# Kernel tuning notes

Hardware: AMD Instinct MI355X
Metric: run time of the kernel (lower is better)

Reference implementation:

```python
import jax, jax.numpy as jnp
import numpy as np
import math


def setup_inputs() -> dict:
    key = jax.random.key(0)
    ks = jax.random.split(key, 5)
    B, C, E = 4, 2048, 1024
    max_len = 2048
    s = 1.0 / math.sqrt(E)
    return {
        "x": jax.random.normal(ks[0], (B, C, E), dtype=jnp.float32),
        "W_q": jax.random.normal(ks[1], (E, E), dtype=jnp.float32) * s,
        "W_k": jax.random.normal(ks[2], (E, E), dtype=jnp.float32) * s,
        "W_v": jax.random.normal(ks[3], (E, E), dtype=jnp.float32) * s,
        "rel_bias": jax.random.normal(ks[4], (2 * max_len - 1, 1), dtype=jnp.float32),
        "max_len": max_len,
    }


def reference(x, W_q, W_k, W_v, rel_bias, max_len):
    B, C, E = x.shape
    # nn.Linear(bias=False): y = x @ W.T
    Q = jnp.einsum("bce,fe->bcf", x, W_q)
    K = jnp.einsum("bce,fe->bcf", x, W_k)
    V = jnp.einsum("bce,fe->bcf", x, W_v)
    scores = jnp.einsum("bqe,bke->bqk", Q, K) / math.sqrt(E)
    pos = jnp.arange(C)
    rel_dist = jnp.clip(pos[None, :] - pos[:, None] + (max_len - 1), 0, 2 * max_len - 2)
    bias = rel_bias[rel_dist, 0]  # [C, C]
    scores = scores + bias[None, :, :]
    weights = jax.nn.softmax(scores, axis=-1)
    out = jnp.einsum("bqk,bke->bqe", weights, V)
    return out, weights
```

## Files before the change

kernel.cpp:

```cpp
#include <hip/hip_runtime.h>
#include <hip/hip_bf16.h>
#include <math.h>

typedef __attribute__((ext_vector_type(8))) short short8;
typedef __attribute__((ext_vector_type(4))) short short4v;
typedef __attribute__((ext_vector_type(4))) float f32x4;

static __device__ __forceinline__ short f2bf(float f) {
  union { float f; unsigned u; } x;
  x.f = f;
  unsigned r = x.u + 0x7fffu + ((x.u >> 16) & 1u);
  return (short)(r >> 16);
}

#define GLD16(g, l)                                                   \
  __builtin_amdgcn_global_load_lds(                                   \
      (const __attribute__((address_space(1))) void*)(g),             \
      (__attribute__((address_space(3))) void*)(l), 16, 0, 0)
#define BAR() asm volatile("s_barrier" ::: "memory")
#define VMCNT6() asm volatile("s_waitcnt vmcnt(6)" ::: "memory")
#define VMCNT0() asm volatile("s_waitcnt vmcnt(0)" ::: "memory")

__global__ __launch_bounds__(256) void cvt_f32_bf16(const float* __restrict__ in,
                                                    short* __restrict__ out, int n8) {
  int i = blockIdx.x * 256 + threadIdx.x;
  if (i >= n8) return;
  const float4* p = (const float4*)in + (size_t)i * 2;
  float4 a = p[0], b = p[1];
  short8 o;
  o[0] = f2bf(a.x); o[1] = f2bf(a.y); o[2] = f2bf(a.z); o[3] = f2bf(a.w);
  o[4] = f2bf(b.x); o[5] = f2bf(b.y); o[6] = f2bf(b.z); o[7] = f2bf(b.w);
  *((short8*)out + i) = o;
}

template <int MODE>
__global__ __launch_bounds__(512) void gemm3b(
    const short* __restrict__ A, const short* __restrict__ Bt,
    void* __restrict__ C0, void* __restrict__ C1, void* __restrict__ C2,
    const float* __restrict__ rel_bias,
    int N, int K, long aZ, long bZ, long cZ, int Cdim, float scale, int ml) {
  __shared__ short sA[3][256 * 64];
  __shared__ short sB[3][128 * 64];
  const int tid = threadIdx.x, lane = tid & 63, wid = tid >> 6;
  const int z = blockIdx.z;
  const short* Az = A + (size_t)z * aZ;
  const short* Bz = Bt + (size_t)z * bZ;
  const int brow = blockIdx.x * 256, bcol = blockIdx.y * 128;
  const int wr = wid >> 2, wc = wid & 3;
  const int lrow = lane & 15, kg = lane >> 4;
  const int l8 = lane >> 3, lm8 = lane & 7;
  const int scol = (lm8 ^ l8) * 8;

  const short* aS[2][2];
  int aD[2][2];
#pragma unroll
  for (int h = 0; h < 2; ++h)
#pragma unroll
    for (int j = 0; j < 2; ++j) {
      int c = wid * 2 + j;
      int rb = c * 8 + (c >= 8 ? 64 : 0) + h * 64;
      aS[h][j] = Az + (size_t)(brow + rb + l8) * K + scol;
      aD[h][j] = rb * 64;
    }
  const short* bS[2];
  int bD[2];
#pragma unroll
  for (int h = 0; h < 2; ++h) {
    int rb = wid * 8 + h * 64;
    bS[h] = Bz + (size_t)(bcol + rb + l8) * K + scol;
    bD[h] = rb * 64;
  }

  const int sks0 = ((0 + kg) ^ (lrow & 7)) * 8;
  const int sks1 = ((4 + kg) ^ (lrow & 7)) * 8;
  const int aR = (wr * 128 + lrow) * 64;
  const int bR = (wc * 32 + lrow) * 64;

  short8 a[4][2], b[2][2];
  f32x4 acc[8][2] = {};

  short *pa0 = &sA[0][0], *pa1 = &sA[1][0], *pa2 = &sA[2][0];
  short *pb0 = &sB[0][0], *pb1 = &sB[1][0], *pb2 = &sB[2][0];

#define STG_A(PA, H, T)                                          \
  do {                                                           \
    GLD16(aS[H][0] + (size_t)(T) * 64, (PA) + aD[H][0]);         \
    GLD16(aS[H][1] + (size_t)(T) * 64, (PA) + aD[H][1]);         \
  } while (0)
#define STG_B(PB, H, T) GLD16(bS[H] + (size_t)(T) * 64, (PB) + bD[H])
#define RD_A(PA, MH)                                                          \
  do {                                                                        \
    _Pragma("unroll") for (int mq = 0; mq < 4; ++mq) {                        \
      a[mq][0] = *(const short8*)&(PA)[aR + (MH)*4096 + mq * 1024 + sks0];    \
      a[mq][1] = *(const short8*)&(PA)[aR + (MH)*4096 + mq * 1024 + sks1];    \
    }                                                                         \
  } while (0)
#define RD_B(PB)                                                   \
  do {                                                             \
    _Pragma("unroll") for (int nq = 0; nq < 2; ++nq) {             \
      b[nq][0] = *(const short8*)&(PB)[bR + nq * 1024 + sks0];     \
      b[nq][1] = *(const short8*)&(PB)[bR + nq * 1024 + sks1];     \
    }                                                              \
  } while (0)
#define MFMA16(MH)                                                            \
  do {                                                                        \
    __builtin_amdgcn_s_setprio(1);                                            \
    _Pragma("unroll") for (int mq = 0; mq < 4; ++mq)                          \
        _Pragma("unroll") for (int nq = 0; nq < 2; ++nq) {                    \
      acc[(MH)*4 + mq][nq] = __builtin_amdgcn_mfma_f32_16x16x32_bf16(         \
          a[mq][0], b[nq][0], acc[(MH)*4 + mq][nq], 0, 0, 0);                 \
      acc[(MH)*4 + mq][nq] = __builtin_amdgcn_mfma_f32_16x16x32_bf16(         \
          a[mq][1], b[nq][1], acc[(MH)*4 + mq][nq], 0, 0, 0);                 \
    }                                                                         \
    __builtin_amdgcn_s_setprio(0);                                            \
  } while (0)

  STG_A(pa0, 0, 0); STG_B(pb0, 0, 0); STG_A(pa0, 1, 0); STG_B(pb0, 1, 0);
  STG_A(pa1, 0, 1); STG_B(pb1, 0, 1); STG_A(pa1, 1, 1); STG_B(pb1, 1, 1);
  VMCNT6();
  BAR();

  const int NT = K >> 6;
  for (int t = 0; t < NT - 2; ++t) {
    RD_A(pa0, 0); RD_B(pb0);
    STG_A(pa2, 0, t + 2); STG_B(pb2, 0, t + 2);
    BAR();
    MFMA16(0);
    BAR();
    RD_A(pa0, 1);
    STG_A(pa2, 1, t + 2); STG_B(pb2, 1, t + 2);
    VMCNT6();
    BAR();
    MFMA16(1);
    BAR();
    short* q;
    q = pa0; pa0 = pa1; pa1 = pa2; pa2 = q;
    q = pb0; pb0 = pb1; pb1 = pb2; pb2 = q;
  }
  RD_A(pa0, 0); RD_B(pb0);
  BAR(); MFMA16(0); BAR();
  RD_A(pa0, 1);
  VMCNT0();
  BAR(); MFMA16(1); BAR();
  RD_A(pa1, 0); RD_B(pb1);
  BAR(); MFMA16(0); BAR();
  RD_A(pa1, 1);
  BAR(); MFMA16(1);

#pragma unroll
  for (int m = 0; m < 8; ++m) {
#pragma unroll
    for (int n = 0; n < 2; ++n) {
#pragma unroll
      for (int r = 0; r < 4; ++r) {
        float v = acc[m][n][r];
        int gr = brow + wr * 128 + m * 16 + kg * 4 + r;
        int gc = bcol + wc * 32 + n * 16 + lrow;
        if constexpr (MODE == 2) {
          int idx = gc - gr + (ml - 1);
          idx = min(max(idx, 0), 2 * ml - 2);
          ((float*)C0 + (size_t)z * cZ)[(size_t)gr * N + gc] =
              v * scale + rel_bias[idx];
        } else if constexpr (MODE == 3) {
          ((float*)C0 + (size_t)z * cZ)[(size_t)gr * N + gc] = v;
        } else {
          int s = gc >> 10, cc = gc & 1023;
          if (s == 0) {
            ((short*)C0)[(size_t)gr * 1024 + cc] = f2bf(v);
          } else if (s == 1) {
            ((short*)C1)[(size_t)gr * 1024 + cc] = f2bf(v);
          } else {
            int b_ = gr / Cdim, c_ = gr % Cdim;
            ((short*)C2)[((size_t)b_ * 1024 + cc) * Cdim + c_] = f2bf(v);
          }
        }
      }
    }
  }
#undef STG_A
#undef STG_B
#undef RD_A
#undef RD_B
#undef MFMA16
}

__global__ __launch_bounds__(256) void softmax_rows(float* __restrict__ w,
                                                    short* __restrict__ wb, int Cd) {
  const size_t row = blockIdx.x;
  float4* p = (float4*)(w + row * (size_t)Cd);
  const int tid = threadIdx.x;
  float4 v0 = p[tid];
  float4 v1 = p[tid + 256];
  float mx = fmaxf(fmaxf(fmaxf(v0.x, v0.y), fmaxf(v0.z, v0.w)),
                   fmaxf(fmaxf(v1.x, v1.y), fmaxf(v1.z, v1.w)));
#pragma unroll
  for (int o = 32; o; o >>= 1) mx = fmaxf(mx, __shfl_xor(mx, o));
  __shared__ float red[8];
  const int wv = tid >> 6;
  if ((tid & 63) == 0) red[wv] = mx;
  __syncthreads();
  mx = fmaxf(fmaxf(red[0], red[1]), fmaxf(red[2], red[3]));
  v0.x = __expf(v0.x - mx); v0.y = __expf(v0.y - mx);
  v0.z = __expf(v0.z - mx); v0.w = __expf(v0.w - mx);
  v1.x = __expf(v1.x - mx); v1.y = __expf(v1.y - mx);
  v1.z = __expf(v1.z - mx); v1.w = __expf(v1.w - mx);
  float s = v0.x + v0.y + v0.z + v0.w + v1.x + v1.y + v1.z + v1.w;
#pragma unroll
  for (int o = 32; o; o >>= 1) s += __shfl_xor(s, o);
  if ((tid & 63) == 0) red[4 + wv] = s;
  __syncthreads();
  s = red[4] + red[5] + red[6] + red[7];
  float inv = 1.0f / s;
  v0.x *= inv; v0.y *= inv; v0.z *= inv; v0.w *= inv;
  v1.x *= inv; v1.y *= inv; v1.z *= inv; v1.w *= inv;
  p[tid] = v0;
  p[tid + 256] = v1;
  short4v b0, b1;
  b0[0] = f2bf(v0.x); b0[1] = f2bf(v0.y); b0[2] = f2bf(v0.z); b0[3] = f2bf(v0.w);
  b1[0] = f2bf(v1.x); b1[1] = f2bf(v1.y); b1[2] = f2bf(v1.z); b1[3] = f2bf(v1.w);
  short* wrow = wb + row * (size_t)Cd;
  *(short4v*)&wrow[tid * 4] = b0;
  *(short4v*)&wrow[1024 + tid * 4] = b1;
}

extern "C" void kernel_launch(void* const* d_in, const int* in_sizes, int n_in,
                              void* d_out, int out_size, void* d_ws, size_t ws_size,
                              hipStream_t stream) {
  const float* x = (const float*)d_in[0];
  const float* Wq = (const float*)d_in[1];
  const float* Wk = (const float*)d_in[2];
  const float* Wv = (const float*)d_in[3];
  const float* rb = (const float*)d_in[4];

  const int E = 1024;
  const int Mt = in_sizes[0] / E;
  const int Cd = out_size / Mt - E;
  const int B = Mt / Cd;
  const int ml = (in_sizes[4] + 1) / 2;
  const float scale = 1.0f / sqrtf((float)E);

  short* xb = (short*)d_ws;
  short* wqb = xb + (size_t)Mt * E;
  short* wkb = wqb + (size_t)E * E;
  short* wvb = wkb + (size_t)E * E;
  short* Qb = wvb + (size_t)E * E;
  short* Kb = Qb + (size_t)Mt * E;
  short* Vt = Kb + (size_t)Mt * E;
  short* wbf = Qb;

  float* outp = (float*)d_out;
  float* wts = outp + (size_t)Mt * E;

  cvt_f32_bf16<<<(Mt * E) / 2048, 256, 0, stream>>>(x, xb, (Mt * E) / 8);
  cvt_f32_bf16<<<(E * E) / 2048, 256, 0, stream>>>(Wq, wqb, (E * E) / 8);
  cvt_f32_bf16<<<(E * E) / 2048, 256, 0, stream>>>(Wk, wkb, (E * E) / 8);
  cvt_f32_bf16<<<(E * E) / 2048, 256, 0, stream>>>(Wv, wvb, (E * E) / 8);

  dim3 blk(512);
  gemm3b<4><<<dim3(Mt / 256, 3 * E / 128, 1), blk, 0, stream>>>(
      xb, wqb, Qb, Kb, Vt, nullptr, 3 * E, E, 0, 0, 0, Cd, 0.f, ml);
  gemm3b<2><<<dim3(Cd / 256, Cd / 128, B), blk, 0, stream>>>(
      Qb, Kb, wts, nullptr, nullptr, rb, Cd, E, (long)Cd * E, (long)Cd * E,
      (long)Cd * Cd, Cd, scale, ml);
  softmax_rows<<<Mt, 256, 0, stream>>>(wts, wbf, Cd);
  gemm3b<3><<<dim3(Cd / 256, E / 128, B), blk, 0, stream>>>(
      wbf, Vt, outp, nullptr, nullptr, nullptr, E, Cd, (long)Cd * Cd,
      (long)E * Cd, (long)Cd * E, Cd, 0.f, ml);
}
```

Before: 209.2 us.

## Fuse input conversions, remap GEMM workgroups per XCD, transpose V separately

Merges the four fp32-to-bf16 conversion launches into one kernel. Remaps the flat workgroup index in the GEMM so that consecutive tiles land on the same XCD, which should improve L2 reuse. The V projection epilogue now writes row-major with coalesced stores instead of scattered transposed stores, and a separate LDS-tiled transpose kernel builds V^T before the final GEMM. This adds one extra launch and an extra read and write of V.

Result: faster. 199.8 us (-4.5%).

```diff
diff --git a/kernel.cpp b/kernel.cpp
--- a/kernel.cpp
+++ b/kernel.cpp
@@ -21,16 +21,24 @@
 #define VMCNT6() asm volatile("s_waitcnt vmcnt(6)" ::: "memory")
 #define VMCNT0() asm volatile("s_waitcnt vmcnt(0)" ::: "memory")
 
-__global__ __launch_bounds__(256) void cvt_f32_bf16(const float* __restrict__ in,
-                                                    short* __restrict__ out, int n8) {
+__global__ __launch_bounds__(256) void cvt_all(
+    const float* __restrict__ x, const float* __restrict__ wq,
+    const float* __restrict__ wk, const float* __restrict__ wv,
+    short* __restrict__ xb, short* __restrict__ wqb,
+    short* __restrict__ wkb, short* __restrict__ wvb, int n0, int n1) {
   int i = blockIdx.x * 256 + threadIdx.x;
-  if (i >= n8) return;
-  const float4* p = (const float4*)in + (size_t)i * 2;
+  const float* src; short* dst; int off;
+  if (i < n0) { src = x; dst = xb; off = i; }
+  else if (i < n0 + n1) { src = wq; dst = wqb; off = i - n0; }
+  else if (i < n0 + 2 * n1) { src = wk; dst = wkb; off = i - n0 - n1; }
+  else if (i < n0 + 3 * n1) { src = wv; dst = wvb; off = i - n0 - 2 * n1; }
+  else return;
+  const float4* p = (const float4*)src + (size_t)off * 2;
   float4 a = p[0], b = p[1];
   short8 o;
   o[0] = f2bf(a.x); o[1] = f2bf(a.y); o[2] = f2bf(a.z); o[3] = f2bf(a.w);
   o[4] = f2bf(b.x); o[5] = f2bf(b.y); o[6] = f2bf(b.z); o[7] = f2bf(b.w);
-  *((short8*)out + i) = o;
+  *((short8*)dst + off) = o;
 }
 
 template <int MODE>
@@ -42,10 +50,20 @@
   __shared__ short sA[3][256 * 64];
   __shared__ short sB[3][128 * 64];
   const int tid = threadIdx.x, lane = tid & 63, wid = tid >> 6;
-  const int z = blockIdx.z;
+
+  const int gx = gridDim.x, gy = gridDim.y;
+  const int nwg = gx * gy * (int)gridDim.z;
+  const int f = ((int)blockIdx.z * gy + (int)blockIdx.y) * gx + (int)blockIdx.x;
+  const int qq = nwg >> 3, rr = nwg & 7;
+  const int xcd = f & 7, pos = f >> 3;
+  const int lg = (xcd < rr ? xcd * (qq + 1) : rr * (qq + 1) + (xcd - rr) * qq) + pos;
+  const int z = lg / (gx * gy);
+  const int rem = lg - z * (gx * gy);
+  const int bx = rem / gy, by = rem - bx * gy;
+
   const short* Az = A + (size_t)z * aZ;
   const short* Bz = Bt + (size_t)z * bZ;
-  const int brow = blockIdx.x * 256, bcol = blockIdx.y * 128;
+  const int brow = bx * 256, bcol = by * 128;
   const int wr = wid >> 2, wc = wid & 3;
   const int lrow = lane & 15, kg = lane >> 4;
   const int l8 = lane >> 3, lm8 = lane & 7;
@@ -165,14 +183,8 @@
           ((float*)C0 + (size_t)z * cZ)[(size_t)gr * N + gc] = v;
         } else {
           int s = gc >> 10, cc = gc & 1023;
-          if (s == 0) {
-            ((short*)C0)[(size_t)gr * 1024 + cc] = f2bf(v);
-          } else if (s == 1) {
-            ((short*)C1)[(size_t)gr * 1024 + cc] = f2bf(v);
-          } else {
-            int b_ = gr / Cdim, c_ = gr % Cdim;
-            ((short*)C2)[((size_t)b_ * 1024 + cc) * Cdim + c_] = f2bf(v);
-          }
+          short* dst = (s == 0) ? (short*)C0 : (s == 1) ? (short*)C1 : (short*)C2;
+          dst[(size_t)gr * 1024 + cc] = f2bf(v);
         }
       }
     }
@@ -182,6 +194,29 @@
 #undef RD_A
 #undef RD_B
 #undef MFMA16
+}
+
+__global__ __launch_bounds__(256) void transpose_v(const short* __restrict__ vin,
+                                                   short* __restrict__ vout,
+                                                   int Cd, int E) {
+  __shared__ short t[64][72];
+  const int c0 = blockIdx.x * 64, e0 = blockIdx.y * 64, b = blockIdx.z;
+  const int tid = threadIdx.x;
+  const int cr = tid >> 2;
+  const int ec = (tid & 3) * 16;
+  const short* src = vin + ((size_t)b * Cd + c0 + cr) * E + e0 + ec;
+  short8 v0 = *(const short8*)src;
+  short8 v1 = *(const short8*)(src + 8);
+#pragma unroll
+  for (int j = 0; j < 8; ++j) t[ec + j][cr] = v0[j];
+#pragma unroll
+  for (int j = 0; j < 8; ++j) t[ec + 8 + j][cr] = v1[j];
+  __syncthreads();
+  const int er = tid >> 2;
+  const int cc = (tid & 3) * 16;
+  short* dst = vout + ((size_t)b * E + e0 + er) * Cd + c0 + cc;
+  *(short8*)dst = *(const short8*)&t[er][cc];
+  *(short8*)(dst + 8) = *(const short8*)&t[er][cc + 8];
 }
 
 __global__ __launch_bounds__(256) void softmax_rows(float* __restrict__ w,
@@ -245,24 +280,25 @@
   short* wvb = wkb + (size_t)E * E;
   short* Qb = wvb + (size_t)E * E;
   short* Kb = Qb + (size_t)Mt * E;
-  short* Vt = Kb + (size_t)Mt * E;
+  short* Vrow = Kb + (size_t)Mt * E;
+  short* Vt = xb;
   short* wbf = Qb;
 
   float* outp = (float*)d_out;
   float* wts = outp + (size_t)Mt * E;
 
-  cvt_f32_bf16<<<(Mt * E) / 2048, 256, 0, stream>>>(x, xb, (Mt * E) / 8);
-  cvt_f32_bf16<<<(E * E) / 2048, 256, 0, stream>>>(Wq, wqb, (E * E) / 8);
-  cvt_f32_bf16<<<(E * E) / 2048, 256, 0, stream>>>(Wk, wkb, (E * E) / 8);
-  cvt_f32_bf16<<<(E * E) / 2048, 256, 0, stream>>>(Wv, wvb, (E * E) / 8);
+  const int n0 = (Mt * E) / 8, n1 = (E * E) / 8;
+  cvt_all<<<(n0 + 3 * n1 + 255) / 256, 256, 0, stream>>>(
+      x, Wq, Wk, Wv, xb, wqb, wkb, wvb, n0, n1);
 
   dim3 blk(512);
   gemm3b<4><<<dim3(Mt / 256, 3 * E / 128, 1), blk, 0, stream>>>(
-      xb, wqb, Qb, Kb, Vt, nullptr, 3 * E, E, 0, 0, 0, Cd, 0.f, ml);
+      xb, wqb, Qb, Kb, Vrow, nullptr, 3 * E, E, 0, 0, 0, Cd, 0.f, ml);
   gemm3b<2><<<dim3(Cd / 256, Cd / 128, B), blk, 0, stream>>>(
       Qb, Kb, wts, nullptr, nullptr, rb, Cd, E, (long)Cd * E, (long)Cd * E,
       (long)Cd * Cd, Cd, scale, ml);
   softmax_rows<<<Mt, 256, 0, stream>>>(wts, wbf, Cd);
+  transpose_v<<<dim3(Cd / 64, E / 64, B), 256, 0, stream>>>(Vrow, Vt, Cd, E);
   gemm3b<3><<<dim3(Cd / 256, E / 128, B), blk, 0, stream>>>(
       wbf, Vt, outp, nullptr, nullptr, nullptr, E, Cd, (long)Cd * Cd,
       (long)E * Cd, (long)Cd * E, Cd, 0.f, ml);
```
